# Kernel optimization log

Measured on AMD Instinct MI355X. Metric: run time of the kernel, lower is better.

## Reference

```python
import jax, jax.numpy as jnp
import numpy as np

HIDDEN = 128
D = 3


def _safe_norm(diff):
    # norm over last axis with NaN-free value at diff==0 (diagonal, masked out later)
    s = jnp.sum(diff * diff, axis=-1, keepdims=True)
    return jnp.sqrt(jnp.where(s > 0, s, 1.0)) * (s > 0)


def setup_inputs() -> dict:
    key = jax.random.key(0)
    ks = jax.random.split(key, 7)
    B, N = 4, 512
    pos_scaled = jax.random.normal(ks[0], (B, N, D), dtype=jnp.float32)
    # edge-MLP params: Linear(2,H) -> SiLU -> Linear(H,H) -> SiLU -> Linear(H,1)
    W1 = jax.random.normal(ks[1], (2, HIDDEN), dtype=jnp.float32) / np.sqrt(2.0)
    b1 = jnp.zeros((HIDDEN,), dtype=jnp.float32)
    W2 = jax.random.normal(ks[2], (HIDDEN, HIDDEN), dtype=jnp.float32) / np.sqrt(HIDDEN)
    b2 = jnp.zeros((HIDDEN,), dtype=jnp.float32)
    W3 = jax.random.normal(ks[3], (HIDDEN, 1), dtype=jnp.float32) / np.sqrt(HIDDEN)
    b3 = jnp.zeros((1,), dtype=jnp.float32)
    return {"pos_scaled": pos_scaled, "W1": W1, "b1": b1, "W2": W2, "b2": b2,
            "W3": W3, "b3": b3}


def reference(pos_scaled, W1, b1, W2, b2, W3, b3):
    B, N, _ = pos_scaled.shape
    diff = pos_scaled[:, :, None, :] - pos_scaled[:, None, :, :]   # [B,N,N,D]
    dist = _safe_norm(diff)                                        # [B,N,N,1]
    dist_safe = jnp.clip(dist, 1e-4, 50.0)
    feat = jnp.concatenate([dist_safe, 1.0 / dist_safe], axis=-1)  # [B,N,N,2]
    h = jax.nn.silu(feat @ W1 + b1)                                # [B,N,N,H]
    h = jax.nn.silu(h @ W2 + b2)                                   # [B,N,N,H]
    mag = h @ W3 + b3                                              # [B,N,N,1]
    mask = (~jnp.eye(N, dtype=bool))[None, :, :, None]
    pair_forces = mag * (diff / jnp.clip(dist, 1e-6, None)) * mask # [B,N,N,D]
    return jnp.sum(pair_forces, axis=2)                            # [B,N,D]
```

## Files before the change

kernel.cpp:

```cpp
#include <hip/hip_runtime.h>

#define H       128
#define NPTS    512
#define NBATCH  4
#define BLOCK   256
#define WAVES   4
#define PW      8

#define TSAMP   8192
#define TIVL    8191
#define T0      (-13.2877123795f)
#define TRANGE  (18.9315685693f)
#define TABLE_FLOATS (2 * TSAMP)
#define TABLE_BYTES  (TABLE_FLOATS * 4u)

__device__ __forceinline__ float fast_rcp(float x) { return __builtin_amdgcn_rcpf(x); }

__device__ __forceinline__ float silu_f(float x) {
    float e = __expf(-x);
    return x * fast_rcp(1.0f + e);
}

__global__ __launch_bounds__(BLOCK) void build_mag_table(
    const float* __restrict__ W1, const float* __restrict__ b1,
    const float* __restrict__ W2, const float* __restrict__ b2,
    const float* __restrict__ W3, const float* __restrict__ b3,
    float* __restrict__ tab)
{
    __shared__ float W2s[H * H];
    __shared__ float W1s[2 * H];
    __shared__ float b1s[H], b2s[H], W3s[H];
    __shared__ float h1s[WAVES][H][PW];

    const int tid  = threadIdx.x;
    const int lane = tid & 63;
    const int w    = tid >> 6;

    {
        const float4* src = (const float4*)W2;
        float4* dst = (float4*)W2s;
        #pragma unroll
        for (int r = 0; r < (H * H / 4) / BLOCK; ++r)
            dst[r * BLOCK + tid] = src[r * BLOCK + tid];
        if (tid < 2 * H) W1s[tid] = W1[tid];
        if (tid < H) { b1s[tid] = b1[tid]; b2s[tid] = b2[tid]; W3s[tid] = W3[tid]; }
    }

    const float b3v = b3[0];
    const int base  = blockIdx.x * (WAVES * PW) + w * PW;

    __syncthreads();

    float d8[PW], in8[PW];
    #pragma unroll
    for (int p = 0; p < PW; ++p) {
        float t  = fmaf((float)(base + p), TRANGE / (float)TIVL, T0);
        float d  = exp2f(t);
        float ds = fminf(fmaxf(d, 1e-4f), 50.0f);
        d8[p]  = ds;
        in8[p] = 1.0f / ds;
    }

    #pragma unroll
    for (int kk = 0; kk < 2; ++kk) {
        const int ch = lane + kk * 64;
        const float wa = W1s[ch], wb = W1s[H + ch], bb = b1s[ch];
        float v[PW];
        #pragma unroll
        for (int p = 0; p < PW; ++p)
            v[p] = silu_f(fmaf(d8[p], wa, fmaf(in8[p], wb, bb)));
        float4* dst = (float4*)&h1s[w][ch][0];
        dst[0] = make_float4(v[0], v[1], v[2], v[3]);
        dst[1] = make_float4(v[4], v[5], v[6], v[7]);
    }

    const int k0 = 2 * lane;
    float acc0[PW], acc1[PW];
    #pragma unroll
    for (int p = 0; p < PW; ++p) { acc0[p] = 0.f; acc1[p] = 0.f; }

    #pragma unroll 4
    for (int j = 0; j < H; ++j) {
        const float4 ha = *(const float4*)&h1s[w][j][0];
        const float4 hb = *(const float4*)&h1s[w][j][4];
        const float2 ww = *(const float2*)&W2s[j * H + k0];
        const float wx = ww.x, wy = ww.y;
        acc0[0] = fmaf(ha.x, wx, acc0[0]); acc1[0] = fmaf(ha.x, wy, acc1[0]);
        acc0[1] = fmaf(ha.y, wx, acc0[1]); acc1[1] = fmaf(ha.y, wy, acc1[1]);
        acc0[2] = fmaf(ha.z, wx, acc0[2]); acc1[2] = fmaf(ha.z, wy, acc1[2]);
        acc0[3] = fmaf(ha.w, wx, acc0[3]); acc1[3] = fmaf(ha.w, wy, acc1[3]);
        acc0[4] = fmaf(hb.x, wx, acc0[4]); acc1[4] = fmaf(hb.x, wy, acc1[4]);
        acc0[5] = fmaf(hb.y, wx, acc0[5]); acc1[5] = fmaf(hb.y, wy, acc1[5]);
        acc0[6] = fmaf(hb.z, wx, acc0[6]); acc1[6] = fmaf(hb.z, wy, acc1[6]);
        acc0[7] = fmaf(hb.w, wx, acc0[7]); acc1[7] = fmaf(hb.w, wy, acc1[7]);
    }

    const float b20 = b2s[k0], b21 = b2s[k0 + 1];
    const float w30 = W3s[k0], w31 = W3s[k0 + 1];
    float part[PW];
    #pragma unroll
    for (int p = 0; p < PW; ++p)
        part[p] = silu_f(acc0[p] + b20) * w30 + silu_f(acc1[p] + b21) * w31;

    #pragma unroll
    for (int off = 32; off >= 1; off >>= 1) {
        #pragma unroll
        for (int p = 0; p < PW; ++p)
            part[p] += __shfl_xor(part[p], off);
    }

    if (lane == 0) {
        #pragma unroll
        for (int p = 0; p < PW; ++p) {
            const int k = base + p;
            const float g = part[p] + b3v;
            if (k < TIVL) tab[2 * k] = g;
            if (k >= 1)   tab[2 * k - 1] = g;
        }
    }
}

__global__ __launch_bounds__(BLOCK) void eval_forces(
    const float* __restrict__ pos, const float* __restrict__ tab,
    float* __restrict__ out)
{
    __shared__ float poss[NPTS * 3];

    const int tid  = threadIdx.x;
    const int lane = tid & 63;
    const int w    = tid >> 6;
    const int row  = blockIdx.x * WAVES + w;
    const int b    = row >> 9;
    const int i    = row & (NPTS - 1);

    {
        const float4* src = (const float4*)(pos + b * NPTS * 3);
        float4* dst = (float4*)poss;
        for (int r = tid; r < NPTS * 3 / 4; r += BLOCK) dst[r] = src[r];
    }
    __syncthreads();

    const float pix = poss[3 * i + 0];
    const float piy = poss[3 * i + 1];
    const float piz = poss[3 * i + 2];

    const float INVH = (float)TIVL / TRANGE;
    const float XOFF = -T0 * ((float)TIVL / TRANGE);
    const float2* tab2 = (const float2*)tab;

    float fx = 0.f, fy = 0.f, fz = 0.f;

    #pragma unroll
    for (int k = 0; k < NPTS / 64; ++k) {
        const int j = lane + 64 * k;
        const float dx = pix - poss[3 * j + 0];
        const float dy = piy - poss[3 * j + 1];
        const float dz = piz - poss[3 * j + 2];
        const float s  = fmaf(dx, dx, fmaf(dy, dy, dz * dz));
        const bool ok  = (s > 0.0f) && (j != i);
        const float rs = __builtin_amdgcn_rsqf(fmaxf(s, 1e-30f));
        const float d  = s * rs;
        const float ds = fminf(fmaxf(d, 1e-4f), 50.0f);
        float x = fmaf(__log2f(ds), INVH, XOFF);
        x = fminf(fmaxf(x, 0.0f), (float)TIVL - 0.001f);
        const int   kk = (int)x;
        const float fr = x - (float)kk;
        const float2 g = tab2[kk];
        const float mag = fmaf(fr, g.y - g.x, g.x);
        const float f   = ok ? mag * fminf(rs, 1e6f) : 0.0f;
        fx = fmaf(f, dx, fx);
        fy = fmaf(f, dy, fy);
        fz = fmaf(f, dz, fz);
    }

    #pragma unroll
    for (int off = 32; off >= 1; off >>= 1) {
        fx += __shfl_xor(fx, off);
        fy += __shfl_xor(fy, off);
        fz += __shfl_xor(fz, off);
    }
    if (lane == 0) {
        out[row * 3 + 0] = fx;
        out[row * 3 + 1] = fy;
        out[row * 3 + 2] = fz;
    }
}

extern "C" void kernel_launch(void* const* d_in, const int* in_sizes, int n_in,
                              void* d_out, int out_size, void* d_ws, size_t ws_size,
                              hipStream_t stream) {
    const float* pos = (const float*)d_in[0];
    const float* W1  = (const float*)d_in[1];
    const float* b1  = (const float*)d_in[2];
    const float* W2  = (const float*)d_in[3];
    const float* b2  = (const float*)d_in[4];
    const float* W3  = (const float*)d_in[5];
    const float* b3  = (const float*)d_in[6];
    float* out = (float*)d_out;
    float* tab = (float*)d_ws;

    hipLaunchKernelGGL(build_mag_table, dim3(TSAMP / (WAVES * PW)), dim3(BLOCK), 0, stream,
                       W1, b1, W2, b2, W3, b3, tab);
    hipLaunchKernelGGL(eval_forces, dim3(NBATCH * NPTS / WAVES), dim3(BLOCK), 0, stream,
                       pos, tab, out);
}
```

Measured before the change: 76.49 us.

## Fuse table build and force evaluation into one cooperative kernel with grid sync

Merges the MLP lookup-table construction and the pairwise force evaluation into a single cooperative kernel of 256 blocks. A grid-wide sync separates the two phases, and the positions are staged into shared memory before the sync. This removes the second kernel launch and the inter-kernel gap. In exchange, each block now handles 8 rows instead of 4 blocks sharing that work, and it adds the cost of a grid barrier and a larger shared-memory footprint (W2s plus poss), which may limit occupancy.

```diff
diff --git a/kernel.cpp b/kernel.cpp
--- a/kernel.cpp
+++ b/kernel.cpp
@@ -1,4 +1,7 @@
 #include <hip/hip_runtime.h>
+#include <hip/hip_cooperative_groups.h>
+
+namespace cg = cooperative_groups;
 
 #define H       128
 #define NPTS    512
@@ -7,12 +10,14 @@
 #define WAVES   4
 #define PW      8
 
+#define NBLK    256
+#define ROWS_PER_BLK  (NBATCH * NPTS / NBLK)
+#define ROWS_PER_WAVE (ROWS_PER_BLK / WAVES)
+
 #define TSAMP   8192
 #define TIVL    8191
 #define T0      (-13.2877123795f)
 #define TRANGE  (18.9315685693f)
-#define TABLE_FLOATS (2 * TSAMP)
-#define TABLE_BYTES  (TABLE_FLOATS * 4u)
 
 __device__ __forceinline__ float fast_rcp(float x) { return __builtin_amdgcn_rcpf(x); }
 
@@ -21,20 +26,31 @@
     return x * fast_rcp(1.0f + e);
 }
 
-__global__ __launch_bounds__(BLOCK) void build_mag_table(
+__global__ __launch_bounds__(BLOCK) void fused_forces(
+    const float* __restrict__ pos,
     const float* __restrict__ W1, const float* __restrict__ b1,
     const float* __restrict__ W2, const float* __restrict__ b2,
     const float* __restrict__ W3, const float* __restrict__ b3,
-    float* __restrict__ tab)
+    float* __restrict__ tab, float* __restrict__ out)
 {
     __shared__ float W2s[H * H];
     __shared__ float W1s[2 * H];
     __shared__ float b1s[H], b2s[H], W3s[H];
     __shared__ float h1s[WAVES][H][PW];
+    __shared__ float poss[NPTS * 3];
 
     const int tid  = threadIdx.x;
     const int lane = tid & 63;
     const int w    = tid >> 6;
+
+    const int row0 = blockIdx.x * ROWS_PER_BLK;
+    const int bb   = row0 >> 9;
+
+    {
+        const float4* src = (const float4*)(pos + bb * NPTS * 3);
+        float4* dst = (float4*)poss;
+        for (int r = tid; r < NPTS * 3 / 4; r += BLOCK) dst[r] = src[r];
+    }
 
     {
         const float4* src = (const float4*)W2;
@@ -64,11 +80,11 @@
     #pragma unroll
     for (int kk = 0; kk < 2; ++kk) {
         const int ch = lane + kk * 64;
-        const float wa = W1s[ch], wb = W1s[H + ch], bb = b1s[ch];
+        const float wa = W1s[ch], wb = W1s[H + ch], bbv = b1s[ch];
         float v[PW];
         #pragma unroll
         for (int p = 0; p < PW; ++p)
-            v[p] = silu_f(fmaf(d8[p], wa, fmaf(in8[p], wb, bb)));
+            v[p] = silu_f(fmaf(d8[p], wa, fmaf(in8[p], wb, bbv)));
         float4* dst = (float4*)&h1s[w][ch][0];
         dst[0] = make_float4(v[0], v[1], v[2], v[3]);
         dst[1] = make_float4(v[4], v[5], v[6], v[7]);
@@ -118,71 +134,58 @@
             if (k >= 1)   tab[2 * k - 1] = g;
         }
     }
-}
-
-__global__ __launch_bounds__(BLOCK) void eval_forces(
-    const float* __restrict__ pos, const float* __restrict__ tab,
-    float* __restrict__ out)
-{
-    __shared__ float poss[NPTS * 3];
-
-    const int tid  = threadIdx.x;
-    const int lane = tid & 63;
-    const int w    = tid >> 6;
-    const int row  = blockIdx.x * WAVES + w;
-    const int b    = row >> 9;
-    const int i    = row & (NPTS - 1);
-
-    {
-        const float4* src = (const float4*)(pos + b * NPTS * 3);
-        float4* dst = (float4*)poss;
-        for (int r = tid; r < NPTS * 3 / 4; r += BLOCK) dst[r] = src[r];
-    }
-    __syncthreads();
-
-    const float pix = poss[3 * i + 0];
-    const float piy = poss[3 * i + 1];
-    const float piz = poss[3 * i + 2];
+
+    cg::this_grid().sync();
 
     const float INVH = (float)TIVL / TRANGE;
     const float XOFF = -T0 * ((float)TIVL / TRANGE);
     const float2* tab2 = (const float2*)tab;
 
-    float fx = 0.f, fy = 0.f, fz = 0.f;
-
-    #pragma unroll
-    for (int k = 0; k < NPTS / 64; ++k) {
-        const int j = lane + 64 * k;
-        const float dx = pix - poss[3 * j + 0];
-        const float dy = piy - poss[3 * j + 1];
-        const float dz = piz - poss[3 * j + 2];
-        const float s  = fmaf(dx, dx, fmaf(dy, dy, dz * dz));
-        const bool ok  = (s > 0.0f) && (j != i);
-        const float rs = __builtin_amdgcn_rsqf(fmaxf(s, 1e-30f));
-        const float d  = s * rs;
-        const float ds = fminf(fmaxf(d, 1e-4f), 50.0f);
-        float x = fmaf(__log2f(ds), INVH, XOFF);
-        x = fminf(fmaxf(x, 0.0f), (float)TIVL - 0.001f);
-        const int   kk = (int)x;
-        const float fr = x - (float)kk;
-        const float2 g = tab2[kk];
-        const float mag = fmaf(fr, g.y - g.x, g.x);
-        const float f   = ok ? mag * fminf(rs, 1e6f) : 0.0f;
-        fx = fmaf(f, dx, fx);
-        fy = fmaf(f, dy, fy);
-        fz = fmaf(f, dz, fz);
-    }
-
-    #pragma unroll
-    for (int off = 32; off >= 1; off >>= 1) {
-        fx += __shfl_xor(fx, off);
-        fy += __shfl_xor(fy, off);
-        fz += __shfl_xor(fz, off);
-    }
-    if (lane == 0) {
-        out[row * 3 + 0] = fx;
-        out[row * 3 + 1] = fy;
-        out[row * 3 + 2] = fz;
+    #pragma unroll
+    for (int rr = 0; rr < ROWS_PER_WAVE; ++rr) {
+        const int row = row0 + w * ROWS_PER_WAVE + rr;
+        const int i   = row & (NPTS - 1);
+
+        const float pix = poss[3 * i + 0];
+        const float piy = poss[3 * i + 1];
+        const float piz = poss[3 * i + 2];
+
+        float fx = 0.f, fy = 0.f, fz = 0.f;
+
+        #pragma unroll
+        for (int k = 0; k < NPTS / 64; ++k) {
+            const int j = lane + 64 * k;
+            const float dx = pix - poss[3 * j + 0];
+            const float dy = piy - poss[3 * j + 1];
+            const float dz = piz - poss[3 * j + 2];
+            const float s  = fmaf(dx, dx, fmaf(dy, dy, dz * dz));
+            const bool ok  = (s > 0.0f) && (j != i);
+            const float rs = __builtin_amdgcn_rsqf(fmaxf(s, 1e-30f));
+            const float d  = s * rs;
+            const float ds = fminf(fmaxf(d, 1e-4f), 50.0f);
+            float x = fmaf(__log2f(ds), INVH, XOFF);
+            x = fminf(fmaxf(x, 0.0f), (float)TIVL - 0.001f);
+            const int   kk = (int)x;
+            const float fr = x - (float)kk;
+            const float2 g = tab2[kk];
+            const float mag = fmaf(fr, g.y - g.x, g.x);
+            const float f   = ok ? mag * fminf(rs, 1e6f) : 0.0f;
+            fx = fmaf(f, dx, fx);
+            fy = fmaf(f, dy, fy);
+            fz = fmaf(f, dz, fz);
+        }
+
+        #pragma unroll
+        for (int off = 32; off >= 1; off >>= 1) {
+            fx += __shfl_xor(fx, off);
+            fy += __shfl_xor(fy, off);
+            fz += __shfl_xor(fz, off);
+        }
+        if (lane == 0) {
+            out[row * 3 + 0] = fx;
+            out[row * 3 + 1] = fy;
+            out[row * 3 + 2] = fz;
+        }
     }
 }
 
@@ -199,8 +202,10 @@
     float* out = (float*)d_out;
     float* tab = (float*)d_ws;
 
-    hipLaunchKernelGGL(build_mag_table, dim3(TSAMP / (WAVES * PW)), dim3(BLOCK), 0, stream,
-                       W1, b1, W2, b2, W3, b3, tab);
-    hipLaunchKernelGGL(eval_forces, dim3(NBATCH * NPTS / WAVES), dim3(BLOCK), 0, stream,
-                       pos, tab, out);
+    void* args[] = {
+        (void*)&pos, (void*)&W1, (void*)&b1, (void*)&W2, (void*)&b2,
+        (void*)&W3, (void*)&b3, (void*)&tab, (void*)&out
+    };
+    hipLaunchCooperativeKernel((const void*)fused_forces,
+                               dim3(NBLK), dim3(BLOCK), args, 0, stream);
 }
```

Result: slower. 120.4 us (+57.3%).
